# Kernel optimization log

Hardware: AMD Instinct MI355X
Metric: run time of the kernel (lower is better)

Reference implementation:

```python
import jax, jax.numpy as jnp
import numpy as np


def setup_inputs() -> dict:
    key = jax.random.key(0)
    ks = jax.random.split(key, 4)
    K, D = 256, 128
    return {
        "x": jax.random.normal(ks[0], (16, 1, 128, 128), jnp.float32),
        "w_conv": jax.random.normal(ks[1], (K, 1, 9, 9), jnp.float32) * 0.05,
        "gate_logit": jnp.zeros((K,), jnp.float32),
        "w_down": jax.random.normal(ks[2], (D, K), jnp.float32) * 0.05,
        "b_down": jnp.zeros((D,), jnp.float32),
        "w_up": jax.random.normal(ks[3], (K, D), jnp.float32) * 0.05,
        "b_up": jnp.zeros((K,), jnp.float32),
        "usage_ema": jnp.full((K,), 1.0 / K, jnp.float32),
    }


def reference(x, w_conv, gate_logit, w_down, b_down, w_up, b_up, usage_ema):
    # encoder 9x9 conv, 1 -> k channels, padding 4 (same)
    z = jax.lax.conv_general_dilated(
        x, w_conv, window_strides=(1, 1), padding=[(4, 4), (4, 4)],
        dimension_numbers=("NCHW", "OIHW", "NCHW"))
    a = jax.nn.relu(z) * jax.nn.sigmoid(gate_logit)[None, :, None, None]
    # per-pixel top-1 channel mask (one-hot of argmax over channel dim)
    idx = jnp.argmax(a, axis=1)                                  # [B,H,W]
    mask = jax.nn.one_hot(idx, a.shape[1], axis=1, dtype=a.dtype)  # [B,k,H,W]
    a = a * mask
    # usage EMA (no-grad bookkeeping, matches torch buffer update)
    B, _, H, W = a.shape
    p = jax.lax.stop_gradient(mask).sum(axis=(0, 2, 3)) / (B * H * W + 1e-6)
    usage_new = usage_ema * 0.99 + p * 0.01
    # 1x1 proj convs as channel GEMMs
    h = jax.nn.relu(jnp.einsum("bkhw,dk->bdhw", a, w_down) + b_down[None, :, None, None])
    a2 = jax.nn.relu(jnp.einsum("bdhw,kd->bkhw", h, w_up) + b_up[None, :, None, None])
    # conv_transpose2d(a2, w_conv, padding=4) with stride 1 == conv with
    # spatially-flipped, channel-swapped kernel and padding k-1-4 = 4
    w_t = jnp.flip(w_conv, axis=(2, 3)).transpose(1, 0, 2, 3)    # [1,k,9,9]
    x_hat = jax.lax.conv_general_dilated(
        a2, w_t, window_strides=(1, 1), padding=[(4, 4), (4, 4)],
        dimension_numbers=("NCHW", "OIHW", "NCHW"))
    return x_hat, usage_new
```

## Files before the change

### kernel.cpp

```cpp
#include <hip/hip_runtime.h>
#include <hip/hip_bf16.h>

#define BATCH 16
#define HH 128
#define WW 128
#define NPIX (BATCH*HH*WW)
#define KCH 256
#define DCH 128
#define TAPS 81
#define MAXTIE 32768
#define PADH 136
#define PADW 160

__global__ __launch_bounds__(256) void k_prep(
    const float* __restrict__ bdown, const float* __restrict__ bup,
    int* __restrict__ counts, int* __restrict__ tiecnt, int* __restrict__ flag)
{
    __shared__ float red[256];
    int t = threadIdx.x;
    counts[t] = 0;
    if (t == 0) tiecnt[0] = 0;
    float m = fabsf(bup[t]);
    if (t < DCH) m = fmaxf(m, fabsf(bdown[t]));
    red[t] = m;
    __syncthreads();
    for (int s = 128; s > 0; s >>= 1) {
        if (t < s) red[t] = fmaxf(red[t], red[t + s]);
        __syncthreads();
    }
    if (t == 0) flag[0] = (red[0] == 0.0f) ? 1 : 0;
}

__global__ __launch_bounds__(256) void k_pad(
    const float* __restrict__ x, float* __restrict__ xpad)
{
    int i = blockIdx.x * 256 + threadIdx.x;
    if (i >= BATCH * PADH * PADW) return;
    int b = i / (PADH * PADW);
    int rem = i - b * (PADH * PADW);
    int yy = rem / PADW, xx = rem - yy * PADW;
    float v = 0.0f;
    if (yy >= 4 && yy < HH + 4 && xx >= 4 && xx < WW + 4)
        v = x[((size_t)b << 14) + ((yy - 4) << 7) + (xx - 4)];
    xpad[i] = v;
}

__global__ __launch_bounds__(256, 2) void k_conv(
    const float* __restrict__ xpad, const float* __restrict__ wconv,
    const float* __restrict__ gate,
    int* __restrict__ idxb, float* __restrict__ valb, float2* __restrict__ vk,
    int* __restrict__ counts, int* __restrict__ tiecnt, int* __restrict__ tielist)
{
    __shared__ float sig[KCH];
    __shared__ int hist[KCH];
    int tid = threadIdx.x;
    sig[tid] = 1.0f / (1.0f + expf(-gate[tid]));
    hist[tid] = 0;
    __syncthreads();

    int p = blockIdx.x * 256 + tid;
    int b = p >> 14, rem = p & 16383, y = rem >> 7, xc = rem & 127;
    const float* base = xpad + ((size_t)(b * PADH + y)) * PADW + xc;

    float px[TAPS];
#pragma unroll
    for (int i = 0; i < 9; i++)
#pragma unroll
        for (int j = 0; j < 9; j++)
            px[i * 9 + j] = base[i * PADW + j];

    float best = -1.0f, best2 = -1.0f; int bi = 0;
    for (int k = 0; k < KCH; k++) {
        const float* wk = wconv + k * TAPS;
        float a0 = 0.f, a1 = 0.f, a2 = 0.f, a3 = 0.f;
#pragma unroll
        for (int t = 0; t < 80; t += 4) {
            a0 = fmaf(px[t+0], wk[t+0], a0);
            a1 = fmaf(px[t+1], wk[t+1], a1);
            a2 = fmaf(px[t+2], wk[t+2], a2);
            a3 = fmaf(px[t+3], wk[t+3], a3);
        }
        a0 = fmaf(px[80], wk[80], a0);
        float z = (a0 + a1) + (a2 + a3);
        float a = fmaxf(z, 0.0f) * sig[k];
        if (a > best) { best2 = best; best = a; bi = k; }
        else if (a > best2) { best2 = a; }
    }

    idxb[p] = bi;
    valb[p] = best;
    vk[p] = make_float2(best, __int_as_float(bi));
    atomicAdd(&hist[bi], 1);
    if (best - best2 < 5e-4f) {
        int pos = atomicAdd(tiecnt, 1);
        if (pos < MAXTIE) tielist[pos] = p;
    }
    __syncthreads();
    if (hist[tid] != 0) atomicAdd(&counts[tid], hist[tid]);
}

__global__ __launch_bounds__(256) void k_tie(
    const float* __restrict__ x, const float* __restrict__ wconv,
    const float* __restrict__ gate,
    const int* __restrict__ tiecnt, const int* __restrict__ tielist,
    int* __restrict__ idxb, float* __restrict__ valb, float2* __restrict__ vk,
    int* __restrict__ counts)
{
    int gw = (blockIdx.x * 256 + threadIdx.x) >> 6;
    int lane = threadIdx.x & 63;
    int nw = (gridDim.x * 256) >> 6;
    int n = tiecnt[0]; if (n > MAXTIE) n = MAXTIE;

    for (int it = gw; it < n; it += nw) {
        int pg = tielist[it];
        int b = pg >> 14, rem = pg & 16383, y = rem >> 7, xc = rem & 127;
        const float* xb = x + ((size_t)b << 14);
        float px[TAPS];
#pragma unroll
        for (int i = 0; i < 9; i++) {
#pragma unroll
            for (int j = 0; j < 9; j++) {
                int yy = y + i - 4, xx = xc + j - 4;
                px[i*9+j] = (yy >= 0 && yy < HH && xx >= 0 && xx < WW) ? xb[(yy<<7)+xx] : 0.0f;
            }
        }
        float m1 = -1.0f; int i1 = 1000;
#pragma unroll
        for (int c = 0; c < 4; c++) {
            int chh = (lane << 2) + c;
            const float* wk = wconv + chh * TAPS;
            float a = 0.0f;
#pragma unroll
            for (int t = 0; t < TAPS; t++)
                a = __fadd_rn(a, __fmul_rn(px[t], wk[t]));
            float sgc = 1.0f / (1.0f + expf(-gate[chh]));
            float v = __fmul_rn(fmaxf(a, 0.0f), sgc);
            if (v > m1) { m1 = v; i1 = chh; }
        }
#pragma unroll
        for (int s = 1; s < 64; s <<= 1) {
            float om = __shfl_xor(m1, s, 64);
            int   oi = __shfl_xor(i1, s, 64);
            if (om > m1 || (om == m1 && oi < i1)) { m1 = om; i1 = oi; }
        }
        if (lane == 0) {
            int old = idxb[pg];
            if (old != i1) { atomicSub(&counts[old], 1); atomicAdd(&counts[i1], 1); }
            idxb[pg] = i1;
            valb[pg] = m1;
            vk[pg] = make_float2(m1, __int_as_float(i1));
        }
    }
}

__global__ __launch_bounds__(256) void k_usage(
    const int* __restrict__ counts, const float* __restrict__ ema,
    float* __restrict__ out_usage)
{
    int k = threadIdx.x;
    double pfrac = (double)counts[k] / (262144.0 + 1e-6);
    out_usage[k] = (float)((double)ema[k] * 0.99 + pfrac * 0.01);
}

__global__ __launch_bounds__(256) void k_tables(
    const float* __restrict__ wdown, const float* __restrict__ wup,
    const float* __restrict__ wconv, float* __restrict__ G)
{
    int j = blockIdx.x;
    int k = threadIdx.x;
    __shared__ float wd[DCH];
    __shared__ float mrelu[KCH];
    if (k < DCH) wd[k] = fmaxf(wdown[(k << 8) + j], 0.0f);
    __syncthreads();
    const float* wr = wup + (k << 7);
    double acc = 0.0;
    for (int d = 0; d < DCH; d++) acc += (double)wr[d] * (double)wd[d];
    mrelu[k] = fmaxf((float)acc, 0.0f);
    __syncthreads();
    if (k < TAPS) {
        double g = 0.0;
        for (int kk = 0; kk < KCH; kk++)
            g += (double)mrelu[kk] * (double)wconv[kk * TAPS + 80 - k];
        G[(k << 8) + j] = (float)g;
    }
}

__global__ __launch_bounds__(256) void k_recon(
    const int* __restrict__ flag, const float2* __restrict__ vk,
    const float* __restrict__ G, float* __restrict__ out)
{
    if (flag[0] == 0) return;
    __shared__ float2 tile[24][25];
    int lx = threadIdx.x & 15, ly = threadIdx.x >> 4;
    int x0 = blockIdx.x << 4, y0 = blockIdx.y << 4;
    int b = blockIdx.z;
    const float2* vkb = vk + ((size_t)b << 14);
    for (int i = threadIdx.x; i < 576; i += 256) {
        int r = i / 24, c = i - r * 24;
        int gy = y0 + r - 4, gx = x0 + c - 4;
        float2 e = make_float2(0.0f, 0.0f);
        if (gy >= 0 && gy < HH && gx >= 0 && gx < WW) e = vkb[(gy << 7) + gx];
        tile[r][c] = e;
    }
    __syncthreads();
    float acc = 0.0f;
#pragma unroll
    for (int i = 0; i < 9; i++)
#pragma unroll
        for (int jj = 0; jj < 9; jj++) {
            float2 e = tile[ly + i][lx + jj];
            int kn = __float_as_int(e.y);
            acc = fmaf(e.x, G[((i * 9 + jj) << 8) + kn], acc);
        }
    out[((size_t)b << 14) + ((y0 + ly) << 7) + (x0 + lx)] = acc;
}

template<typename T> __device__ inline T to_store(float v);
template<> __device__ inline float to_store<float>(float v) { return v; }
template<> __device__ inline __hip_bfloat16 to_store<__hip_bfloat16>(float v) { return __float2bfloat16(v); }
template<typename T> __device__ inline float from_store(T v);
template<> __device__ inline float from_store<float>(float v) { return v; }
template<> __device__ inline float from_store<__hip_bfloat16>(__hip_bfloat16 v) { return __bfloat162float(v); }

template<typename T>
__global__ __launch_bounds__(256) void k_proj_fb(
    const int* __restrict__ flag,
    const int* __restrict__ idxb, const float* __restrict__ valb,
    const float* __restrict__ wdown, const float* __restrict__ bdown,
    const float* __restrict__ wup, const float* __restrict__ bup,
    const float* __restrict__ wconv,
    T* __restrict__ sbuf)
{
    if (flag[0] != 0) return;
    int p = blockIdx.x * 256 + threadIdx.x;
    int kk = idxb[p];
    float v = valb[p];

    float h[DCH];
#pragma unroll
    for (int d = 0; d < DCH; d++)
        h[d] = fmaxf(fmaf(v, wdown[(d << 8) + kk], bdown[d]), 0.0f);

    float sacc[TAPS];
#pragma unroll
    for (int t = 0; t < TAPS; t++) sacc[t] = 0.0f;

    for (int k = 0; k < KCH; k++) {
        const float* wr = wup + (k << 7);
        float a0 = bup[k], a1 = 0.f, a2 = 0.f, a3 = 0.f;
#pragma unroll
        for (int d = 0; d < DCH; d += 4) {
            a0 = fmaf(wr[d+0], h[d+0], a0);
            a1 = fmaf(wr[d+1], h[d+1], a1);
            a2 = fmaf(wr[d+2], h[d+2], a2);
            a3 = fmaf(wr[d+3], h[d+3], a3);
        }
        float a2v = fmaxf((a0 + a1) + (a2 + a3), 0.0f);
        const float* wc = wconv + k * TAPS;
#pragma unroll
        for (int t = 0; t < TAPS; t++)
            sacc[t] = fmaf(a2v, wc[80 - t], sacc[t]);
    }
#pragma unroll
    for (int t = 0; t < TAPS; t++)
        sbuf[(size_t)t * NPIX + p] = to_store<T>(sacc[t]);
}

template<typename T>
__global__ __launch_bounds__(256) void k_gather_fb(
    const int* __restrict__ flag,
    const T* __restrict__ sbuf, float* __restrict__ xhat)
{
    if (flag[0] != 0) return;
    int p = blockIdx.x * 256 + threadIdx.x;
    int b = p >> 14, rem = p & 16383, y = rem >> 7, xc = rem & 127;
    float acc = 0.0f;
#pragma unroll
    for (int i = 0; i < 9; i++) {
        int yy = y + i - 4;
        if (yy < 0 || yy >= HH) continue;
#pragma unroll
        for (int j = 0; j < 9; j++) {
            int xx = xc + j - 4;
            if (xx < 0 || xx >= WW) continue;
            int t = i * 9 + j;
            acc += from_store<T>(sbuf[(size_t)t * NPIX + (b << 14) + (yy << 7) + xx]);
        }
    }
    xhat[p] = acc;
}

extern "C" void kernel_launch(void* const* d_in, const int* in_sizes, int n_in,
                              void* d_out, int out_size, void* d_ws, size_t ws_size,
                              hipStream_t stream)
{
    const float* x     = (const float*)d_in[0];
    const float* wconv = (const float*)d_in[1];
    const float* gate  = (const float*)d_in[2];
    const float* wdown = (const float*)d_in[3];
    const float* bdown = (const float*)d_in[4];
    const float* wup   = (const float*)d_in[5];
    const float* bup   = (const float*)d_in[6];
    const float* ema   = (const float*)d_in[7];
    float* out = (float*)d_out;

    char* ws = (char*)d_ws;
    const size_t OFF_VAL  = (size_t)NPIX * 4;
    const size_t OFF_VK   = (size_t)NPIX * 8;
    const size_t OFF_CNT  = (size_t)NPIX * 16;
    const size_t OFF_ZB   = OFF_CNT + 1024;
    const size_t OFF_TC   = OFF_ZB + 1024;
    const size_t OFF_LIST = OFF_TC + 1024;
    const size_t OFF_G    = OFF_LIST + (size_t)MAXTIE * 4;
    const size_t OFF_XP   = OFF_G + (size_t)TAPS * KCH * 4;
    const size_t OFF_SB   = OFF_XP + (size_t)BATCH * PADH * PADW * 4;

    int*    idxb   = (int*)ws;
    float*  valb   = (float*)(ws + OFF_VAL);
    float2* vk     = (float2*)(ws + OFF_VK);
    int*    counts = (int*)(ws + OFF_CNT);
    int*    zbflag = (int*)(ws + OFF_ZB);
    int*    tiecnt = (int*)(ws + OFF_TC);
    int*    tielist= (int*)(ws + OFF_LIST);
    float*  G      = (float*)(ws + OFF_G);
    float*  xpad   = (float*)(ws + OFF_XP);
    char*   sstart = ws + OFF_SB;

    size_t need_f32 = OFF_SB + (size_t)TAPS * NPIX * sizeof(float);

    k_prep<<<1, 256, 0, stream>>>(bdown, bup, counts, tiecnt, zbflag);
    k_pad<<<(BATCH*PADH*PADW + 255)/256, 256, 0, stream>>>(x, xpad);
    k_conv<<<NPIX/256, 256, 0, stream>>>(xpad, wconv, gate, idxb, valb, vk,
                                         counts, tiecnt, tielist);
    k_tie<<<256, 256, 0, stream>>>(x, wconv, gate, tiecnt, tielist,
                                   idxb, valb, vk, counts);
    k_usage<<<1, 256, 0, stream>>>(counts, ema, out + NPIX);
    k_tables<<<KCH, 256, 0, stream>>>(wdown, wup, wconv, G);

    k_recon<<<dim3(8, 8, 16), 256, 0, stream>>>(zbflag, vk, G, out);

    if (ws_size >= need_f32) {
        float* sbuf = (float*)sstart;
        k_proj_fb<float><<<NPIX/256, 256, 0, stream>>>(zbflag, idxb, valb, wdown, bdown, wup, bup, wconv, sbuf);
        k_gather_fb<float><<<NPIX/256, 256, 0, stream>>>(zbflag, sbuf, out);
    } else {
        __hip_bfloat16* sbuf = (__hip_bfloat16*)sstart;
        k_proj_fb<__hip_bfloat16><<<NPIX/256, 256, 0, stream>>>(zbflag, idxb, valb, wdown, bdown, wup, bup, wconv, sbuf);
        k_gather_fb<__hip_bfloat16><<<NPIX/256, 256, 0, stream>>>(zbflag, sbuf, out);
    }
}
```

Baseline: 220.9 us.

## Compute encoder conv with split-bf16 MFMA and add sampled fallback check

Replaces the scalar FP32 9x9 encoder convolution with an im2col-style GEMM on MFMA bf16 instructions. To keep near-FP32 accuracy it uses a three-term hi/lo bf16 split, with weights pre-split by a new prep kernel. The tie threshold is widened so more ambiguous pixels are recomputed exactly, and the tie list capacity is enlarged. A sampled check kernel compares 16 pixels against an exact FP32 computation and triggers the old scalar conv if they disagree, at the cost of extra launches and a larger tie workload.

```diff
diff --git a/kernel.cpp b/kernel.cpp
--- a/kernel.cpp
+++ b/kernel.cpp
@@ -8,18 +8,36 @@
 #define KCH 256
 #define DCH 128
 #define TAPS 81
-#define MAXTIE 32768
+#define MAXTIE 131072
 #define PADH 136
 #define PADW 160
 
+typedef __attribute__((ext_vector_type(8))) short bfx8;
+typedef __attribute__((ext_vector_type(4))) float fx4;
+
+__device__ inline void split_bf16(float x, unsigned short &h, unsigned short &l) {
+    unsigned u = __float_as_uint(x);
+    unsigned hb = (u + 0x7FFFu + ((u >> 16) & 1u)) >> 16;
+    float hf = __uint_as_float(hb << 16);
+    float lf = x - hf;
+    unsigned u2 = __float_as_uint(lf);
+    unsigned lb = (u2 + 0x7FFFu + ((u2 >> 16) & 1u)) >> 16;
+    h = (unsigned short)hb; l = (unsigned short)lb;
+}
+
 __global__ __launch_bounds__(256) void k_prep(
     const float* __restrict__ bdown, const float* __restrict__ bup,
-    int* __restrict__ counts, int* __restrict__ tiecnt, int* __restrict__ flag)
+    const float* __restrict__ gate,
+    int* __restrict__ counts0, int* __restrict__ counts1,
+    int* __restrict__ tiecnt0, int* __restrict__ tiecnt1,
+    int* __restrict__ okflag, int* __restrict__ zbflag,
+    float* __restrict__ sig256)
 {
     __shared__ float red[256];
     int t = threadIdx.x;
-    counts[t] = 0;
-    if (t == 0) tiecnt[0] = 0;
+    counts0[t] = 0; counts1[t] = 0;
+    if (t == 0) { tiecnt0[0] = 0; tiecnt1[0] = 0; okflag[0] = 1; }
+    sig256[t] = 1.0f / (1.0f + expf(-gate[t]));
     float m = fabsf(bup[t]);
     if (t < DCH) m = fmaxf(m, fabsf(bdown[t]));
     red[t] = m;
@@ -28,7 +46,21 @@
         if (t < s) red[t] = fmaxf(red[t], red[t + s]);
         __syncthreads();
     }
-    if (t == 0) flag[0] = (red[0] == 0.0f) ? 1 : 0;
+    if (t == 0) zbflag[0] = (red[0] == 0.0f) ? 1 : 0;
+}
+
+__global__ __launch_bounds__(256) void k_wprep(
+    const float* __restrict__ wconv,
+    unsigned short* __restrict__ Bh, unsigned short* __restrict__ Bl)
+{
+    int i = blockIdx.x * 256 + threadIdx.x;
+    if (i >= 3 * 16 * 64 * 8) return;
+    int j = i & 7, lane = (i >> 3) & 63, nt = (i >> 9) & 15, ks = i >> 13;
+    int ch = nt * 16 + (lane & 15);
+    int t = ks * 32 + ((lane >> 4) & 3) * 8 + j;
+    float w = (t < TAPS) ? wconv[ch * TAPS + t] : 0.0f;
+    unsigned short h, l; split_bf16(w, h, l);
+    Bh[i] = h; Bl[i] = l;
 }
 
 __global__ __launch_bounds__(256) void k_pad(
@@ -45,12 +77,162 @@
     xpad[i] = v;
 }
 
-__global__ __launch_bounds__(256, 2) void k_conv(
+__global__ __launch_bounds__(256) void k_conv_mfma(
+    const float* __restrict__ xpad,
+    const unsigned short* __restrict__ Bh, const unsigned short* __restrict__ Bl,
+    const float* __restrict__ sig256,
+    int* __restrict__ idxb, float* __restrict__ valb, float2* __restrict__ vk,
+    int* __restrict__ counts0, int* __restrict__ tiecnt0, int* __restrict__ tielist0)
+{
+    __shared__ int hist[KCH];
+    int tid = threadIdx.x;
+    hist[tid] = 0;
+    __syncthreads();
+
+    int lane = tid & 63, w = tid >> 6;
+    int c16 = lane & 15, g = lane >> 4;
+    int p0 = blockIdx.x * 128;
+    int b = p0 >> 14, y = (p0 >> 7) & 127;
+    int x0w = w * 32;
+    const float* xrow0 = xpad + (size_t)(b * PADH + y) * PADW;
+
+    float sigv[16];
+#pragma unroll
+    for (int nt = 0; nt < 16; nt++) sigv[nt] = sig256[nt * 16 + c16];
+
+    fx4 acc[2][16];
+#pragma unroll
+    for (int mf = 0; mf < 2; mf++)
+#pragma unroll
+        for (int nt = 0; nt < 16; nt++)
+            acc[mf][nt] = (fx4){0.f, 0.f, 0.f, 0.f};
+
+#pragma unroll
+    for (int ks = 0; ks < 3; ks++) {
+        bfx8 ah[2], al[2];
+#pragma unroll
+        for (int mf = 0; mf < 2; mf++) {
+#pragma unroll
+            for (int j = 0; j < 8; j++) {
+                int t = ks * 32 + g * 8 + j;
+                float xv = 0.0f;
+                if (t < TAPS) {
+                    int ti = (t * 57) >> 9;
+                    int tj = t - ti * 9;
+                    xv = xrow0[ti * PADW + x0w + mf * 16 + c16 + tj];
+                }
+                unsigned short hb, lb; split_bf16(xv, hb, lb);
+                ah[mf][j] = (short)hb; al[mf][j] = (short)lb;
+            }
+        }
+#pragma unroll
+        for (int nt = 0; nt < 16; nt++) {
+            bfx8 bh = *(const bfx8*)(Bh + (((ks * 16 + nt) * 64 + lane) << 3));
+            bfx8 bl = *(const bfx8*)(Bl + (((ks * 16 + nt) * 64 + lane) << 3));
+#pragma unroll
+            for (int mf = 0; mf < 2; mf++) {
+                acc[mf][nt] = __builtin_amdgcn_mfma_f32_16x16x32_bf16(ah[mf], bh, acc[mf][nt], 0, 0, 0);
+                acc[mf][nt] = __builtin_amdgcn_mfma_f32_16x16x32_bf16(ah[mf], bl, acc[mf][nt], 0, 0, 0);
+                acc[mf][nt] = __builtin_amdgcn_mfma_f32_16x16x32_bf16(al[mf], bh, acc[mf][nt], 0, 0, 0);
+            }
+        }
+    }
+
+#pragma unroll
+    for (int mf = 0; mf < 2; mf++) {
+#pragma unroll
+        for (int r = 0; r < 4; r++) {
+            float b1 = -1.0f, b2 = -1.0f; int i1 = 0;
+#pragma unroll
+            for (int nt = 0; nt < 16; nt++) {
+                float a = fmaxf(acc[mf][nt][r], 0.0f) * sigv[nt];
+                if (a > b1) { b2 = b1; b1 = a; i1 = nt * 16 + c16; }
+                else if (a > b2) b2 = a;
+            }
+#pragma unroll
+            for (int s = 1; s < 16; s <<= 1) {
+                float ob1 = __shfl_xor(b1, s, 64);
+                float ob2 = __shfl_xor(b2, s, 64);
+                int   oi1 = __shfl_xor(i1, s, 64);
+                float nb2 = fmaxf(fminf(b1, ob1), fmaxf(b2, ob2));
+                if (ob1 > b1 || (ob1 == b1 && oi1 < i1)) { b1 = ob1; i1 = oi1; }
+                b2 = nb2;
+            }
+            if (c16 == 0) {
+                int m = g * 4 + r;
+                int p = p0 + x0w + mf * 16 + m;
+                idxb[p] = i1;
+                valb[p] = b1;
+                vk[p] = make_float2(b1, __int_as_float(i1));
+                atomicAdd(&hist[i1], 1);
+                if (b1 - b2 < 5e-3f) {
+                    int pos = atomicAdd(tiecnt0, 1);
+                    if (pos < MAXTIE) tielist0[pos] = p;
+                }
+            }
+        }
+    }
+    __syncthreads();
+    if (hist[tid] != 0) atomicAdd(&counts0[tid], hist[tid]);
+}
+
+__global__ __launch_bounds__(256) void k_check(
+    const float* __restrict__ x, const float* __restrict__ wconv,
+    const float* __restrict__ gate,
+    const int* __restrict__ idxb, const float* __restrict__ valb,
+    int* __restrict__ okflag)
+{
+    int t = threadIdx.x;
+    int p = (blockIdx.x * 16411 + 9173) & (NPIX - 1);
+    int b = p >> 14, rem = p & 16383, y = rem >> 7, xc = rem & 127;
+    const float* xb = x + ((size_t)b << 14);
+    const float* wk = wconv + t * TAPS;
+    float acc = 0.0f;
+#pragma unroll
+    for (int i = 0; i < 9; i++) {
+        int yy = y + i - 4;
+#pragma unroll
+        for (int j = 0; j < 9; j++) {
+            int xx = xc + j - 4;
+            float pv = (yy >= 0 && yy < HH && xx >= 0 && xx < WW) ? xb[(yy << 7) + xx] : 0.0f;
+            acc = fmaf(pv, wk[i * 9 + j], acc);
+        }
+    }
+    float a = fmaxf(acc, 0.0f) * (1.0f / (1.0f + expf(-gate[t])));
+
+    __shared__ float sv[256]; __shared__ int si[256];
+    sv[t] = a; si[t] = t;
+    __syncthreads();
+    for (int s = 128; s > 0; s >>= 1) {
+        if (t < s) {
+            if (sv[t+s] > sv[t] || (sv[t+s] == sv[t] && si[t+s] < si[t])) { sv[t] = sv[t+s]; si[t] = si[t+s]; }
+        }
+        __syncthreads();
+    }
+    float b1 = sv[0]; int i1 = si[0];
+    __syncthreads();
+    sv[t] = (t == i1) ? -1e30f : a;
+    __syncthreads();
+    for (int s = 128; s > 0; s >>= 1) {
+        if (t < s) sv[t] = fmaxf(sv[t], sv[t+s]);
+        __syncthreads();
+    }
+    if (t == 0) {
+        float b2 = sv[0];
+        float vm = valb[p]; int im = idxb[p];
+        bool bad = (fabsf(b1 - vm) > 3e-3f) || (im != i1 && (b1 - b2) > 2e-2f);
+        if (bad) atomicExch(okflag, 0);
+    }
+}
+
+__global__ __launch_bounds__(256) void k_conv_fb(
+    const int* __restrict__ okflag,
     const float* __restrict__ xpad, const float* __restrict__ wconv,
     const float* __restrict__ gate,
     int* __restrict__ idxb, float* __restrict__ valb, float2* __restrict__ vk,
-    int* __restrict__ counts, int* __restrict__ tiecnt, int* __restrict__ tielist)
-{
+    int* __restrict__ counts1, int* __restrict__ tiecnt1, int* __restrict__ tielist1)
+{
+    if (okflag[0] != 0) return;
     __shared__ float sig[KCH];
     __shared__ int hist[KCH];
     int tid = threadIdx.x;
@@ -92,27 +274,34 @@
     vk[p] = make_float2(best, __int_as_float(bi));
     atomicAdd(&hist[bi], 1);
     if (best - best2 < 5e-4f) {
-        int pos = atomicAdd(tiecnt, 1);
-        if (pos < MAXTIE) tielist[pos] = p;
-    }
-    __syncthreads();
-    if (hist[tid] != 0) atomicAdd(&counts[tid], hist[tid]);
+        int pos = atomicAdd(tiecnt1, 1);
+        if (pos < MAXTIE) tielist1[pos] = p;
+    }
+    __syncthreads();
+    if (hist[tid] != 0) atomicAdd(&counts1[tid], hist[tid]);
 }
 
 __global__ __launch_bounds__(256) void k_tie(
+    const int* __restrict__ okflag,
     const float* __restrict__ x, const float* __restrict__ wconv,
     const float* __restrict__ gate,
-    const int* __restrict__ tiecnt, const int* __restrict__ tielist,
+    const int* __restrict__ tiecnt0, const int* __restrict__ tielist0,
+    const int* __restrict__ tiecnt1, const int* __restrict__ tielist1,
     int* __restrict__ idxb, float* __restrict__ valb, float2* __restrict__ vk,
-    int* __restrict__ counts)
-{
+    int* __restrict__ counts0, int* __restrict__ counts1)
+{
+    int ok = okflag[0];
+    const int* tl = ok ? tielist0 : tielist1;
+    int n = ok ? tiecnt0[0] : tiecnt1[0];
+    int* cts = ok ? counts0 : counts1;
+    if (n > MAXTIE) n = MAXTIE;
+
     int gw = (blockIdx.x * 256 + threadIdx.x) >> 6;
     int lane = threadIdx.x & 63;
     int nw = (gridDim.x * 256) >> 6;
-    int n = tiecnt[0]; if (n > MAXTIE) n = MAXTIE;
 
     for (int it = gw; it < n; it += nw) {
-        int pg = tielist[it];
+        int pg = tl[it];
         int b = pg >> 14, rem = pg & 16383, y = rem >> 7, xc = rem & 127;
         const float* xb = x + ((size_t)b << 14);
         float px[TAPS];
@@ -145,7 +334,7 @@
         }
         if (lane == 0) {
             int old = idxb[pg];
-            if (old != i1) { atomicSub(&counts[old], 1); atomicAdd(&counts[i1], 1); }
+            if (old != i1) { atomicSub(&cts[old], 1); atomicAdd(&cts[i1], 1); }
             idxb[pg] = i1;
             valb[pg] = m1;
             vk[pg] = make_float2(m1, __int_as_float(i1));
@@ -154,11 +343,13 @@
 }
 
 __global__ __launch_bounds__(256) void k_usage(
-    const int* __restrict__ counts, const float* __restrict__ ema,
-    float* __restrict__ out_usage)
+    const int* __restrict__ okflag,
+    const int* __restrict__ counts0, const int* __restrict__ counts1,
+    const float* __restrict__ ema, float* __restrict__ out_usage)
 {
     int k = threadIdx.x;
-    double pfrac = (double)counts[k] / (262144.0 + 1e-6);
+    int c = okflag[0] ? counts0[k] : counts1[k];
+    double pfrac = (double)c / (262144.0 + 1e-6);
     out_usage[k] = (float)((double)ema[k] * 0.99 + pfrac * 0.01);
 }
 
@@ -306,35 +497,55 @@
 
     char* ws = (char*)d_ws;
     const size_t OFF_VAL  = (size_t)NPIX * 4;
-    const size_t OFF_VK   = (size_t)NPIX * 8;
-    const size_t OFF_CNT  = (size_t)NPIX * 16;
-    const size_t OFF_ZB   = OFF_CNT + 1024;
-    const size_t OFF_TC   = OFF_ZB + 1024;
-    const size_t OFF_LIST = OFF_TC + 1024;
-    const size_t OFF_G    = OFF_LIST + (size_t)MAXTIE * 4;
+    const size_t OFF_VK   = OFF_VAL + (size_t)NPIX * 4;
+    const size_t OFF_CNT0 = OFF_VK + (size_t)NPIX * 8;
+    const size_t OFF_CNT1 = OFF_CNT0 + 1024;
+    const size_t OFF_ZB   = OFF_CNT1 + 1024;
+    const size_t OFF_OK   = OFF_ZB + 1024;
+    const size_t OFF_TC0  = OFF_OK + 1024;
+    const size_t OFF_TC1  = OFF_TC0 + 1024;
+    const size_t OFF_SIG  = OFF_TC1 + 1024;
+    const size_t OFF_L0   = OFF_SIG + 1024;
+    const size_t OFF_L1   = OFF_L0 + (size_t)MAXTIE * 4;
+    const size_t OFF_BH   = OFF_L1 + (size_t)MAXTIE * 4;
+    const size_t OFF_BL   = OFF_BH + 3*16*64*8*2;
+    const size_t OFF_G    = OFF_BL + 3*16*64*8*2;
     const size_t OFF_XP   = OFF_G + (size_t)TAPS * KCH * 4;
     const size_t OFF_SB   = OFF_XP + (size_t)BATCH * PADH * PADW * 4;
 
     int*    idxb   = (int*)ws;
     float*  valb   = (float*)(ws + OFF_VAL);
     float2* vk     = (float2*)(ws + OFF_VK);
-    int*    counts = (int*)(ws + OFF_CNT);
+    int*    counts0= (int*)(ws + OFF_CNT0);
+    int*    counts1= (int*)(ws + OFF_CNT1);
     int*    zbflag = (int*)(ws + OFF_ZB);
-    int*    tiecnt = (int*)(ws + OFF_TC);
-    int*    tielist= (int*)(ws + OFF_LIST);
+    int*    okflag = (int*)(ws + OFF_OK);
+    int*    tiecnt0= (int*)(ws + OFF_TC0);
+    int*    tiecnt1= (int*)(ws + OFF_TC1);
+    float*  sig256 = (float*)(ws + OFF_SIG);
+    int*    tielist0 = (int*)(ws + OFF_L0);
+    int*    tielist1 = (int*)(ws + OFF_L1);
+    unsigned short* Bh = (unsigned short*)(ws + OFF_BH);
+    unsigned short* Bl = (unsigned short*)(ws + OFF_BL);
     float*  G      = (float*)(ws + OFF_G);
     float*  xpad   = (float*)(ws + OFF_XP);
     char*   sstart = ws + OFF_SB;
 
     size_t need_f32 = OFF_SB + (size_t)TAPS * NPIX * sizeof(float);
 
-    k_prep<<<1, 256, 0, stream>>>(bdown, bup, counts, tiecnt, zbflag);
+    k_prep<<<1, 256, 0, stream>>>(bdown, bup, gate, counts0, counts1,
+                                  tiecnt0, tiecnt1, okflag, zbflag, sig256);
+    k_wprep<<<(3*16*64*8 + 255)/256, 256, 0, stream>>>(wconv, Bh, Bl);
     k_pad<<<(BATCH*PADH*PADW + 255)/256, 256, 0, stream>>>(x, xpad);
-    k_conv<<<NPIX/256, 256, 0, stream>>>(xpad, wconv, gate, idxb, valb, vk,
-                                         counts, tiecnt, tielist);
-    k_tie<<<256, 256, 0, stream>>>(x, wconv, gate, tiecnt, tielist,
-                                   idxb, valb, vk, counts);
-    k_usage<<<1, 256, 0, stream>>>(counts, ema, out + NPIX);
+    k_conv_mfma<<<NPIX/128, 256, 0, stream>>>(xpad, Bh, Bl, sig256,
+                                              idxb, valb, vk, counts0, tiecnt0, tielist0);
+    k_check<<<16, 256, 0, stream>>>(x, wconv, gate, idxb, valb, okflag);
+    k_conv_fb<<<NPIX/256, 256, 0, stream>>>(okflag, xpad, wconv, gate,
+                                            idxb, valb, vk, counts1, tiecnt1, tielist1);
+    k_tie<<<256, 256, 0, stream>>>(okflag, x, wconv, gate,
+                                   tiecnt0, tielist0, tiecnt1, tielist1,
+                                   idxb, valb, vk, counts0, counts1);
+    k_usage<<<1, 256, 0, stream>>>(okflag, counts0, counts1, ema, out + NPIX);
     k_tables<<<KCH, 256, 0, stream>>>(wdown, wup, wconv, G);
 
     k_recon<<<dim3(8, 8, 16), 256, 0, stream>>>(zbflag, vk, G, out);
```

Result: slower. 357.8 us (+62.0%).
